# Optimization experiments

Hardware: AMD Instinct MI355X
Metric: run time of the kernel (lower is better)

## Reference

```python
import jax, jax.numpy as jnp
import numpy as np

B, S, D, H = 2, 2048, 2048, 16
DH = D // H  # 128


def _rope(x, cos, sin):
    # Faithful to the source: x is (B, H, S, Dh) (already transposed), and the
    # original apply_rotary_emb slices freqs_cis[:, :H, :] and broadcasts over
    # the S axis -> rotation angle depends on head index (source quirk).
    h = x.shape[1]
    c = cos[:, :h, :][:, :, None, :]  # (1, H, 1, Dh/2)
    s = sin[:, :h, :][:, :, None, :]
    half = x.shape[-1] // 2
    re, im = x[..., :half], x[..., half:]
    return jnp.concatenate([re * c - im * s, re * s + im * c], axis=-1)


def setup_inputs() -> dict:
    key = jax.random.key(0)
    k0, k1, k2 = jax.random.split(key, 3)
    x = jax.random.normal(k0, (B, S, D), jnp.float32)
    Wqkv = jax.random.normal(k1, (D, 3 * D), jnp.float32) / np.float32(np.sqrt(D))
    bqkv = jnp.zeros((3 * D,), jnp.float32)
    Wout = jax.random.normal(k2, (D, D), jnp.float32) / np.float32(np.sqrt(D))
    bout = jnp.zeros((D,), jnp.float32)
    # standard RoPE frequency table, stored as cos/sin (unit-modulus complex)
    inv_freq = 1.0 / (10000.0 ** (np.arange(0, DH // 2, dtype=np.float32) / (DH // 2)))
    ang = np.outer(np.arange(S, dtype=np.float32), inv_freq)  # (S, Dh/2)
    freqs_cos = jnp.asarray(np.cos(ang)[None], jnp.float32)   # (1, S, Dh/2)
    freqs_sin = jnp.asarray(np.sin(ang)[None], jnp.float32)
    mask = jnp.triu(jnp.ones((S, S), bool), 1)[None, None]    # causal, True = masked
    return {"x": x, "Wqkv": Wqkv, "bqkv": bqkv, "Wout": Wout, "bout": bout,
            "freqs_cos": freqs_cos, "freqs_sin": freqs_sin, "mask": mask}


def reference(x, Wqkv, bqkv, Wout, bout, freqs_cos, freqs_sin, mask):
    b, s, d = x.shape
    scale = DH ** (-0.5)
    qkv = x @ Wqkv + bqkv                                   # (B, S, 3D)
    q, k, v = jnp.split(qkv, 3, axis=-1)
    to_heads = lambda t: t.reshape(b, s, H, DH).transpose(0, 2, 1, 3)  # (B,H,S,Dh)
    q, k, v = to_heads(q), to_heads(k), to_heads(v)
    q = _rope(q, freqs_cos, freqs_sin)
    k = _rope(k, freqs_cos, freqs_sin)
    scores = jnp.einsum('bhqd,bhkd->bhqk', q, k) * scale
    scores = jnp.where(mask, -jnp.inf, scores)
    p = jax.nn.softmax(scores, axis=-1)                     # dropout p=0 (eval)
    out = jnp.einsum('bhqk,bhkd->bhqd', p, v)
    out = out.transpose(0, 2, 1, 3).reshape(b, s, d)
    return out @ Wout + bout
```

## Files before the change

kernel.cpp:

```cpp
#include <hip/hip_runtime.h>

#define S_ 2048
#define D_ 2048
#define H_ 16
#define DH_ 128

typedef __attribute__((ext_vector_type(8))) short short8;
typedef __attribute__((ext_vector_type(4))) float f32x4;
typedef __attribute__((ext_vector_type(8))) unsigned short ushort8;
typedef __attribute__((ext_vector_type(4))) unsigned short ushort4v;

__device__ __forceinline__ unsigned short f2bf(float f) {
  unsigned int u;
  __builtin_memcpy(&u, &f, 4);
  unsigned int lsb = (u >> 16) & 1u;
  u += 0x7fffu + lsb;
  return (unsigned short)(u >> 16);
}

__device__ __forceinline__ void gload_lds16(const void* g, void* l) {
  __builtin_amdgcn_global_load_lds(
      (const __attribute__((address_space(1))) unsigned int*)g,
      (__attribute__((address_space(3))) unsigned int*)l, 16, 0, 0);
}

template <int N> __device__ __forceinline__ void vmwait() {
  if constexpr (N == 8)      asm volatile("s_waitcnt vmcnt(8)" ::: "memory");
  else if constexpr (N == 6) asm volatile("s_waitcnt vmcnt(6)" ::: "memory");
  else if constexpr (N == 4) asm volatile("s_waitcnt vmcnt(4)" ::: "memory");
  else if constexpr (N == 3) asm volatile("s_waitcnt vmcnt(3)" ::: "memory");
  else if constexpr (N == 2) asm volatile("s_waitcnt vmcnt(2)" ::: "memory");
  else                       asm volatile("s_waitcnt vmcnt(0)" ::: "memory");
}

#define FENCE_ asm volatile("" ::: "memory")
#define BAR_ { FENCE_; __builtin_amdgcn_s_barrier(); FENCE_; }

__global__ void k_convert_x(const float* __restrict__ x, unsigned short* __restrict__ xb) {
  int idx = blockIdx.x * 256 + threadIdx.x;
  const float4* xv = (const float4*)x;
  float4 a = xv[(size_t)idx * 2];
  float4 b = xv[(size_t)idx * 2 + 1];
  ushort8 o;
  o[0] = f2bf(a.x); o[1] = f2bf(a.y); o[2] = f2bf(a.z); o[3] = f2bf(a.w);
  o[4] = f2bf(b.x); o[5] = f2bf(b.y); o[6] = f2bf(b.z); o[7] = f2bf(b.w);
  *(ushort8*)(xb + (size_t)idx * 8) = o;
}

__global__ void k_prep_w(const float* __restrict__ W, const float* __restrict__ cosb,
                         const float* __restrict__ sinb, unsigned short* __restrict__ WT,
                         int Nw, int rot_limit) {
  __shared__ float tile[32][129];
  const int t = threadIdx.x;
  const int kt = blockIdx.x * 32, nt = blockIdx.y * 128;
#pragma unroll
  for (int i = 0; i < 4; ++i) {
    int q = i * 256 + t;
    int kl = q >> 5, cq = q & 31;
    float4 v = *(const float4*)(W + (size_t)(kt + kl) * Nw + nt + cq * 4);
    tile[kl][cq * 4 + 0] = v.x; tile[kl][cq * 4 + 1] = v.y;
    tile[kl][cq * 4 + 2] = v.z; tile[kl][cq * 4 + 3] = v.w;
  }
  __syncthreads();
  const bool rot = nt < rot_limit;
#pragma unroll
  for (int i = 0; i < 16; ++i) {
    int f = i * 256 + t;
    int kl = f & 31, nl = f >> 5;
    int ng = nt + nl;
    float val;
    if (rot) {
      int i0 = nl & 63;
      int h = (ng & 2047) >> 7;
      float c = cosb[h * 64 + i0], sn = sinb[h * 64 + i0];
      float re = tile[kl][i0], im = tile[kl][i0 + 64];
      val = (nl < 64) ? (re * c - im * sn) : (re * sn + im * c);
    } else {
      val = tile[kl][nl];
    }
    WT[(size_t)ng * 2048 + kt + kl] = f2bf(val);
  }
}

template <int NF, int MODE>
__global__ __launch_bounds__(512, 2) void k_ms(
    const unsigned short* __restrict__ A, const unsigned short* __restrict__ Bt,
    const float* __restrict__ bias,
    unsigned short* __restrict__ Qb, unsigned short* __restrict__ Kb,
    unsigned short* __restrict__ Vt, float* __restrict__ Co) {
  constexpr int BN = NF * 64;
  constexpr int NT = 32;
  constexpr int BBASE = 65536;
  constexpr int BSZ = BN * 128;
  __shared__ unsigned char lds[BBASE + 3 * BSZ];

  const int tid = threadIdx.x, l = tid & 63, w = tid >> 6;
  const int wm = w >> 2, wn = w & 3;
  const int nwg = gridDim.x;
  const int bid = blockIdx.x;
  const int swz = (bid & 7) * (nwg >> 3) + (bid >> 3);
  const int tm = (swz & 15) * 256;
  const int tn = (swz >> 4) * BN;

  const int sslot = (l & 7) ^ (l >> 3);
  const unsigned short* aB = A + (size_t)(tm + (l >> 3)) * 2048 + sslot * 8;
  const unsigned short* bB = Bt + (size_t)(tn + (l >> 3)) * 2048 + sslot * 8;
  const int xg = ((l >> 4) ^ (l & 7)) << 4;
  const int afo = (wm * 128 + (l & 15)) * 128 + xg;
  const int bfo = (wn * (NF * 16) + (l & 15)) * 128 + xg;

  f32x4 acc[8][NF] = {};
  short8 af[8], bf[2 * NF];

#define SAF_(ab_, u_) {                                                         \
  _Pragma("unroll") for (int i_ = 0; i_ < 4; ++i_) {                            \
    int c_ = w + i_ * 8;                                                        \
    gload_lds16(aB + (size_t)(c_ * 8) * 2048 + (u_) * 64,                       \
                lds + (ab_) + c_ * 1024); } }
#define SBF_(bs_, u_) {                                                         \
  _Pragma("unroll") for (int i_ = 0; i_ < NF; ++i_) {                           \
    int c_ = w + i_ * 8;                                                        \
    gload_lds16(bB + (size_t)(c_ * 8) * 2048 + (u_) * 64,                       \
                lds + (bs_) + c_ * 1024); } }

#define RDA2_(ab_, mh_) {                                                       \
  _Pragma("unroll") for (int m_ = 0; m_ < 4; ++m_) {                            \
    unsigned a_ = (ab_) + afo + ((mh_) * 4 + m_) * 2048;                        \
    af[m_]     = *(const short8*)(lds + a_);                                    \
    af[4 + m_] = *(const short8*)(lds + (a_ ^ 64)); } }
#define RDB2_(bb_) {                                                            \
  _Pragma("unroll") for (int n_ = 0; n_ < NF; ++n_) {                           \
    unsigned a_ = (bb_) + bfo + n_ * 2048;                                      \
    bf[n_]      = *(const short8*)(lds + a_);                                   \
    bf[NF + n_] = *(const short8*)(lds + (a_ ^ 64)); } }

#define MMF_(mh_) { __builtin_amdgcn_s_setprio(1);                              \
  _Pragma("unroll") for (int kk_ = 0; kk_ < 2; ++kk_)                           \
  _Pragma("unroll") for (int m_ = 0; m_ < 4; ++m_)                              \
  _Pragma("unroll") for (int n_ = 0; n_ < NF; ++n_)                             \
    acc[(mh_) * 4 + m_][n_] = __builtin_amdgcn_mfma_f32_16x16x32_bf16(          \
        af[kk_ * 4 + m_], bf[kk_ * NF + n_], acc[(mh_) * 4 + m_][n_], 0, 0, 0); \
  __builtin_amdgcn_s_setprio(0); }

  SAF_(0u, 0); SBF_(BBASE, 0); SBF_(BBASE + BSZ, 1);
  vmwait<NF>(); BAR_;

  int bcur = 0, bstg = 2;
#pragma unroll 1
  for (int v = 0; v < NT; ++v) {
    const unsigned ab = (unsigned)(v & 1) * 32768u;
    const unsigned an = (unsigned)((v + 1) & 1) * 32768u;
    const unsigned bb = BBASE + (unsigned)bcur * BSZ;
    const unsigned bs = BBASE + (unsigned)bstg * BSZ;
    RDB2_(bb);
    RDA2_(ab, 0);
    if (v + 1 < NT) SAF_(an, v + 1);
    MMF_(0);
    RDA2_(ab, 1);
    if (v + 2 < NT) SBF_(bs, v + 2);
    MMF_(1);
    if (v < NT - 2) { vmwait<NF>(); } else { vmwait<0>(); }
    BAR_;
    bcur = (bcur == 2) ? 0 : bcur + 1;
    bstg = (bstg == 2) ? 0 : bstg + 1;
  }
#undef SAF_
#undef SBF_
#undef RDA2_
#undef RDB2_
#undef MMF_

  const int ln = l & 15, rb4 = (l >> 4) << 2;
#pragma unroll
  for (int m = 0; m < 8; ++m) {
    int rbase = tm + wm * 128 + m * 16 + rb4;
#pragma unroll
    for (int n = 0; n < NF; ++n) {
      int colg = tn + wn * (NF * 16) + n * 16 + ln;
      float bv = bias[colg];
      if constexpr (MODE == 0) {
        int reg = colg >> 11;
        int h = (colg & 2047) >> 7, dh = colg & 127;
        if (reg == 2) {
          int b = rbase >> 11, s = rbase & 2047;
          ushort4v o;
#pragma unroll
          for (int j = 0; j < 4; ++j) o[j] = f2bf(acc[m][n][j] + bv);
          *(ushort4v*)(Vt + ((size_t)(b * H_ + h) * DH_ + dh) * S_ + s) = o;
        } else {
#pragma unroll
          for (int j = 0; j < 4; ++j) {
            int r = rbase + j;
            int b = r >> 11, s = r & 2047;
            size_t off = ((size_t)(b * H_ + h) * S_ + s) * DH_ + dh;
            float v = acc[m][n][j] + bv;
            if (reg == 0) Qb[off] = f2bf(v * 0.08838834764831845f);
            else Kb[off] = f2bf(v);
          }
        }
      } else {
#pragma unroll
        for (int j = 0; j < 4; ++j)
          Co[(size_t)(rbase + j) * 2048 + colg] = acc[m][n][j] + bv;
      }
    }
  }
}

__global__ __launch_bounds__(256) void k_attn(
    const unsigned short* __restrict__ Qb, const unsigned short* __restrict__ Kb,
    const unsigned short* __restrict__ Vt, unsigned short* __restrict__ Ob) {
  __shared__ unsigned short kls[2][8192];
  __shared__ unsigned short vls[2][8192];
  __shared__ unsigned short pls[4096];
  const int t = threadIdx.x, l = t & 63, w = t >> 6;
  const int pairi = blockIdx.x, bh = blockIdx.y;
  const int b = bh >> 4, h = bh & 15;
  const int rb = (l >> 4) << 2;
  const unsigned short* Qp = Qb + (size_t)bh * S_ * DH_;
  const unsigned short* Kp = Kb + (size_t)bh * S_ * DH_;
  const unsigned short* Vp = Vt + (size_t)bh * DH_ * S_;

#pragma unroll 1
  for (int half = 0; half < 2; ++half) {
    const int qt = half ? (31 - pairi) : pairi;
    const int qb = qt * 64;

    short8 qf[4];
    {
      int row = qb + w * 16 + (l & 15);
#pragma unroll
      for (int c = 0; c < 4; ++c)
        qf[c] = *(const short8*)(Qp + (size_t)row * 128 + c * 32 + ((l >> 4) * 8));
    }

    f32x4 o[8] = {};
    float mrow[4] = {-1e30f, -1e30f, -1e30f, -1e30f};
    float lrow[4] = {0.f, 0.f, 0.f, 0.f};

#pragma unroll
    for (int i = 0; i < 4; ++i) {
      int cid = w + i * 4;
      int krow = cid * 4 + (l >> 4);
      int kslot = (l & 15) ^ (krow & 7);
      gload_lds16(Kp + (size_t)krow * 128 + kslot * 8, &kls[0][cid * 512]);
      int vrow = cid * 8 + (l >> 3);
      int vslot = (l & 7) ^ (vrow & 7);
      gload_lds16(Vp + (size_t)vrow * S_ + vslot * 8, &vls[0][cid * 512]);
    }
    __syncthreads();

#pragma unroll 1
    for (int kvt = 0; kvt <= qt; ++kvt) {
      const int kvb = kvt * 64;
      const int cur = kvt & 1;

      if (kvt < qt) {
        const int kvb2 = kvb + 64;
#pragma unroll
        for (int i = 0; i < 4; ++i) {
          int cid = w + i * 4;
          int krow = cid * 4 + (l >> 4);
          int kslot = (l & 15) ^ (krow & 7);
          gload_lds16(Kp + (size_t)(kvb2 + krow) * 128 + kslot * 8,
                      &kls[cur ^ 1][cid * 512]);
          int vrow = cid * 8 + (l >> 3);
          int vslot = (l & 7) ^ (vrow & 7);
          gload_lds16(Vp + (size_t)vrow * S_ + kvb2 + vslot * 8,
                      &vls[cur ^ 1][cid * 512]);
        }
      }

      f32x4 sc[4];
      __builtin_amdgcn_s_setprio(1);
#pragma unroll
      for (int nb = 0; nb < 4; ++nb) {
        f32x4 sacc = {};
#pragma unroll
        for (int c = 0; c < 4; ++c) {
          int row = nb * 16 + (l & 15);
          int off = (c * 64 + ((l >> 4) * 16)) ^ ((row & 7) << 4);
          short8 kf = *(const short8*)((const char*)kls[cur] + row * 256 + off);
          sacc = __builtin_amdgcn_mfma_f32_16x16x32_bf16(qf[c], kf, sacc, 0, 0, 0);
        }
        sc[nb] = sacc;
      }
      __builtin_amdgcn_s_setprio(0);

      float xs[4][4], xm[4];
      const bool diag = (kvt == qt);
#pragma unroll
      for (int j = 0; j < 4; ++j) {
        float m0 = -1e30f;
#pragma unroll
        for (int nb = 0; nb < 4; ++nb) {
          float x = sc[nb][j];
          if (diag) {
            int kv = kvb + nb * 16 + (l & 15);
            if (kv > qb + w * 16 + rb + j) x = -1e30f;
          }
          xs[j][nb] = x;
          m0 = fmaxf(m0, x);
        }
        xm[j] = m0;
      }
#pragma unroll
      for (int msk = 8; msk >= 1; msk >>= 1)
#pragma unroll
        for (int j = 0; j < 4; ++j) xm[j] = fmaxf(xm[j], __shfl_xor(xm[j], msk));

      bool grow = false;
#pragma unroll
      for (int j = 0; j < 4; ++j) grow |= (xm[j] > mrow[j] + 8.f);
      if (__any(grow)) {
        float fsc[4];
#pragma unroll
        for (int j = 0; j < 4; ++j) {
          float nm = fmaxf(mrow[j], xm[j]);
          fsc[j] = __expf(mrow[j] - nm);
          mrow[j] = nm;
        }
#pragma unroll
        for (int d = 0; d < 8; ++d) {
          o[d][0] *= fsc[0]; o[d][1] *= fsc[1]; o[d][2] *= fsc[2]; o[d][3] *= fsc[3];
        }
#pragma unroll
        for (int j = 0; j < 4; ++j) lrow[j] *= fsc[j];
      }
      float rs[4];
#pragma unroll
      for (int j = 0; j < 4; ++j) {
        float s = 0.f;
#pragma unroll
        for (int nb = 0; nb < 4; ++nb) {
          float p = __expf(xs[j][nb] - mrow[j]);
          xs[j][nb] = p;
          s += p;
        }
        rs[j] = s;
      }
#pragma unroll
      for (int msk = 8; msk >= 1; msk >>= 1)
#pragma unroll
        for (int j = 0; j < 4; ++j) rs[j] += __shfl_xor(rs[j], msk);
#pragma unroll
      for (int j = 0; j < 4; ++j) lrow[j] += rs[j];

#pragma unroll
      for (int j = 0; j < 4; ++j) {
        int prow = rb + j;
#pragma unroll
        for (int nb = 0; nb < 4; ++nb) {
          int colb = (nb * 16 + (l & 15)) * 2;
          *(unsigned short*)((char*)pls + w * 2048 + prow * 128 +
                             (colb ^ ((prow & 7) << 4))) = f2bf(xs[j][nb]);
        }
      }
      __syncthreads();

      __builtin_amdgcn_s_setprio(1);
#pragma unroll
      for (int kc = 0; kc < 2; ++kc) {
        int prow = l & 15;
        int poff = (kc * 64 + ((l >> 4) * 16)) ^ ((prow & 7) << 4);
        short8 pa = *(const short8*)((const char*)pls + w * 2048 + prow * 128 + poff);
#pragma unroll
        for (int d = 0; d < 8; ++d) {
          int vrow = d * 16 + (l & 15);
          int voff = (kc * 64 + ((l >> 4) * 16)) ^ ((vrow & 7) << 4);
          short8 vf = *(const short8*)((const char*)vls[cur] + vrow * 128 + voff);
          o[d] = __builtin_amdgcn_mfma_f32_16x16x32_bf16(pa, vf, o[d], 0, 0, 0);
        }
      }
      __builtin_amdgcn_s_setprio(0);
      __syncthreads();
    }

    float inv[4];
#pragma unroll
    for (int j = 0; j < 4; ++j) inv[j] = 1.f / lrow[j];
#pragma unroll
    for (int d = 0; d < 8; ++d) {
#pragma unroll
      for (int j = 0; j < 4; ++j) {
        int s = qb + w * 16 + rb + j;
        int col = h * 128 + d * 16 + (l & 15);
        Ob[((size_t)(b * S_ + s)) * D_ + col] = f2bf(o[d][j] * inv[j]);
      }
    }
  }
}

extern "C" void kernel_launch(void* const* d_in, const int* in_sizes, int n_in,
                              void* d_out, int out_size, void* d_ws, size_t ws_size,
                              hipStream_t stream) {
  const float* x    = (const float*)d_in[0];
  const float* Wqkv = (const float*)d_in[1];
  const float* bqkv = (const float*)d_in[2];
  const float* Wout = (const float*)d_in[3];
  const float* bout = (const float*)d_in[4];
  const float* fcos = (const float*)d_in[5];
  const float* fsin = (const float*)d_in[6];
  float* out = (float*)d_out;

  char* ws = (char*)d_ws;
  unsigned short* xbf   = (unsigned short*)(ws);
  unsigned short* wqkvT = (unsigned short*)(ws + 16777216);
  unsigned short* woutT = (unsigned short*)(ws + 41943040);
  unsigned short* Qb    = (unsigned short*)(ws + 50331648);
  unsigned short* Kb    = Qb + 8388608;
  unsigned short* Vtb   = Kb + 8388608;
  unsigned short* Ob    = xbf;

  hipLaunchKernelGGL(k_convert_x, dim3(4096), dim3(256), 0, stream, x, xbf);
  hipLaunchKernelGGL(k_prep_w, dim3(64, 48), dim3(256), 0, stream,
                     Wqkv, fcos, fsin, wqkvT, 6144, 4096);
  hipLaunchKernelGGL(k_prep_w, dim3(64, 16), dim3(256), 0, stream,
                     Wout, fcos, fsin, woutT, 2048, 0);
  hipLaunchKernelGGL((k_ms<3, 0>), dim3(512), dim3(512), 0, stream,
                     xbf, wqkvT, bqkv, Qb, Kb, Vtb, (float*)nullptr);
  hipLaunchKernelGGL(k_attn, dim3(16, 32), dim3(256), 0, stream, Qb, Kb, Vtb, Ob);
  hipLaunchKernelGGL((k_ms<2, 1>), dim3(256), dim3(512), 0, stream,
                     Ob, woutT, bout, (unsigned short*)nullptr,
                     (unsigned short*)nullptr, (unsigned short*)nullptr, out);
}
```

Before: 278.0 us.

## Transpose attention score MFMA so each lane owns one query row

After: 249.6 us. -10.2%, faster.

```diff
diff --git a/kernel.cpp b/kernel.cpp
--- a/kernel.cpp
+++ b/kernel.cpp
@@ -122,7 +122,6 @@
     int c_ = w + i_ * 8;                                                        \
     gload_lds16(bB + (size_t)(c_ * 8) * 2048 + (u_) * 64,                       \
                 lds + (bs_) + c_ * 1024); } }
-
 #define RDA2_(ab_, mh_) {                                                       \
   _Pragma("unroll") for (int m_ = 0; m_ < 4; ++m_) {                            \
     unsigned a_ = (ab_) + afo + ((mh_) * 4 + m_) * 2048;                        \
@@ -133,7 +132,6 @@
     unsigned a_ = (bb_) + bfo + n_ * 2048;                                      \
     bf[n_]      = *(const short8*)(lds + a_);                                   \
     bf[NF + n_] = *(const short8*)(lds + (a_ ^ 64)); } }
-
 #define MMF_(mh_) { __builtin_amdgcn_s_setprio(1);                              \
   _Pragma("unroll") for (int kk_ = 0; kk_ < 2; ++kk_)                           \
   _Pragma("unroll") for (int m_ = 0; m_ < 4; ++m_)                              \
@@ -214,9 +212,11 @@
   __shared__ unsigned short vls[2][8192];
   __shared__ unsigned short pls[4096];
   const int t = threadIdx.x, l = t & 63, w = t >> 6;
-  const int pairi = blockIdx.x, bh = blockIdx.y;
+  const int id = blockIdx.x;
+  const int pairi = id >> 5, bh = id & 31;
   const int b = bh >> 4, h = bh & 15;
-  const int rb = (l >> 4) << 2;
+  const int lq = l & 15, lg = l >> 4;
+  const int rb = lg << 2;
   const unsigned short* Qp = Qb + (size_t)bh * S_ * DH_;
   const unsigned short* Kp = Kb + (size_t)bh * S_ * DH_;
   const unsigned short* Vp = Vt + (size_t)bh * DH_ * S_;
@@ -225,18 +225,15 @@
   for (int half = 0; half < 2; ++half) {
     const int qt = half ? (31 - pairi) : pairi;
     const int qb = qt * 64;
+    const int qrow = qb + w * 16 + lq;
 
     short8 qf[4];
-    {
-      int row = qb + w * 16 + (l & 15);
-#pragma unroll
-      for (int c = 0; c < 4; ++c)
-        qf[c] = *(const short8*)(Qp + (size_t)row * 128 + c * 32 + ((l >> 4) * 8));
-    }
+#pragma unroll
+    for (int c = 0; c < 4; ++c)
+      qf[c] = *(const short8*)(Qp + (size_t)qrow * 128 + c * 32 + lg * 8);
 
     f32x4 o[8] = {};
-    float mrow[4] = {-1e30f, -1e30f, -1e30f, -1e30f};
-    float lrow[4] = {0.f, 0.f, 0.f, 0.f};
+    float m = -1e30f, lsum = 0.f;
 
 #pragma unroll
     for (int i = 0; i < 4; ++i) {
@@ -278,96 +275,73 @@
         f32x4 sacc = {};
 #pragma unroll
         for (int c = 0; c < 4; ++c) {
-          int row = nb * 16 + (l & 15);
-          int off = (c * 64 + ((l >> 4) * 16)) ^ ((row & 7) << 4);
+          int row = nb * 16 + lq;
+          int off = (c * 64 + (lg * 16)) ^ ((row & 7) << 4);
           short8 kf = *(const short8*)((const char*)kls[cur] + row * 256 + off);
-          sacc = __builtin_amdgcn_mfma_f32_16x16x32_bf16(qf[c], kf, sacc, 0, 0, 0);
+          sacc = __builtin_amdgcn_mfma_f32_16x16x32_bf16(kf, qf[c], sacc, 0, 0, 0);
         }
         sc[nb] = sacc;
       }
       __builtin_amdgcn_s_setprio(0);
 
-      float xs[4][4], xm[4];
+      float xs[4][4];
+      float xm = -1e30f;
       const bool diag = (kvt == qt);
 #pragma unroll
-      for (int j = 0; j < 4; ++j) {
-        float m0 = -1e30f;
-#pragma unroll
-        for (int nb = 0; nb < 4; ++nb) {
-          float x = sc[nb][j];
-          if (diag) {
-            int kv = kvb + nb * 16 + (l & 15);
-            if (kv > qb + w * 16 + rb + j) x = -1e30f;
-          }
-          xs[j][nb] = x;
-          m0 = fmaxf(m0, x);
-        }
-        xm[j] = m0;
-      }
-#pragma unroll
-      for (int msk = 8; msk >= 1; msk >>= 1)
-#pragma unroll
-        for (int j = 0; j < 4; ++j) xm[j] = fmaxf(xm[j], __shfl_xor(xm[j], msk));
-
-      bool grow = false;
-#pragma unroll
-      for (int j = 0; j < 4; ++j) grow |= (xm[j] > mrow[j] + 8.f);
-      if (__any(grow)) {
-        float fsc[4];
-#pragma unroll
-        for (int j = 0; j < 4; ++j) {
-          float nm = fmaxf(mrow[j], xm[j]);
-          fsc[j] = __expf(mrow[j] - nm);
-          mrow[j] = nm;
-        }
+      for (int nb = 0; nb < 4; ++nb)
+#pragma unroll
+        for (int r = 0; r < 4; ++r) {
+          float x = sc[nb][r];
+          if (diag && (kvb + nb * 16 + rb + r > qrow)) x = -1e30f;
+          xs[nb][r] = x;
+          xm = fmaxf(xm, x);
+        }
+      xm = fmaxf(xm, __shfl_xor(xm, 16));
+      xm = fmaxf(xm, __shfl_xor(xm, 32));
+
+      if (__any(xm > m + 8.f)) {
+        float nm = fmaxf(m, xm);
+        float f = __expf(m - nm);
+        m = nm; lsum *= f;
+        float fj[4];
+#pragma unroll
+        for (int j = 0; j < 4; ++j) fj[j] = __shfl(f, (l & 48) | (rb + j));
 #pragma unroll
         for (int d = 0; d < 8; ++d) {
-          o[d][0] *= fsc[0]; o[d][1] *= fsc[1]; o[d][2] *= fsc[2]; o[d][3] *= fsc[3];
-        }
-#pragma unroll
-        for (int j = 0; j < 4; ++j) lrow[j] *= fsc[j];
-      }
-      float rs[4];
-#pragma unroll
-      for (int j = 0; j < 4; ++j) {
-        float s = 0.f;
-#pragma unroll
-        for (int nb = 0; nb < 4; ++nb) {
-          float p = __expf(xs[j][nb] - mrow[j]);
-          xs[j][nb] = p;
+          o[d][0] *= fj[0]; o[d][1] *= fj[1]; o[d][2] *= fj[2]; o[d][3] *= fj[3];
+        }
+      }
+      float s = 0.f;
+#pragma unroll
+      for (int nb = 0; nb < 4; ++nb)
+#pragma unroll
+        for (int r = 0; r < 4; ++r) {
+          float p = __expf(xs[nb][r] - m);
+          xs[nb][r] = p;
           s += p;
         }
-        rs[j] = s;
-      }
-#pragma unroll
-      for (int msk = 8; msk >= 1; msk >>= 1)
-#pragma unroll
-        for (int j = 0; j < 4; ++j) rs[j] += __shfl_xor(rs[j], msk);
-#pragma unroll
-      for (int j = 0; j < 4; ++j) lrow[j] += rs[j];
-
-#pragma unroll
-      for (int j = 0; j < 4; ++j) {
-        int prow = rb + j;
-#pragma unroll
-        for (int nb = 0; nb < 4; ++nb) {
-          int colb = (nb * 16 + (l & 15)) * 2;
-          *(unsigned short*)((char*)pls + w * 2048 + prow * 128 +
-                             (colb ^ ((prow & 7) << 4))) = f2bf(xs[j][nb]);
-        }
-      }
-      __syncthreads();
+      s += __shfl_xor(s, 16);
+      s += __shfl_xor(s, 32);
+      lsum += s;
+
+#pragma unroll
+      for (int nb = 0; nb < 4; ++nb) {
+        ushort4v pw;
+#pragma unroll
+        for (int r = 0; r < 4; ++r) pw[r] = f2bf(xs[nb][r]);
+        *(ushort4v*)((char*)pls + w * 2048 + lq * 128 +
+                     ((nb * 32 + lg * 8) ^ ((lq & 7) << 4))) = pw;
+      }
 
       __builtin_amdgcn_s_setprio(1);
 #pragma unroll
       for (int kc = 0; kc < 2; ++kc) {
-        int prow = l & 15;
-        int poff = (kc * 64 + ((l >> 4) * 16)) ^ ((prow & 7) << 4);
-        short8 pa = *(const short8*)((const char*)pls + w * 2048 + prow * 128 + poff);
+        short8 pa = *(const short8*)((const char*)pls + w * 2048 + lq * 128 +
+                                     ((kc * 64 + lg * 16) ^ ((lq & 7) << 4)));
 #pragma unroll
         for (int d = 0; d < 8; ++d) {
-          int vrow = d * 16 + (l & 15);
-          int voff = (kc * 64 + ((l >> 4) * 16)) ^ ((vrow & 7) << 4);
+          int vrow = d * 16 + lq;
+          int voff = (kc * 64 + (lg * 16)) ^ ((vrow & 7) << 4);
           short8 vf = *(const short8*)((const char*)vls[cur] + vrow * 128 + voff);
           o[d] = __builtin_amdgcn_mfma_f32_16x16x32_bf16(pa, vf, o[d], 0, 0, 0);
         }
@@ -376,16 +350,17 @@
       __syncthreads();
     }
 
-    float inv[4];
-#pragma unroll
-    for (int j = 0; j < 4; ++j) inv[j] = 1.f / lrow[j];
+    float inv = 1.f / lsum;
+    float invj[4];
+#pragma unroll
+    for (int j = 0; j < 4; ++j) invj[j] = __shfl(inv, (l & 48) | (rb + j));
 #pragma unroll
     for (int d = 0; d < 8; ++d) {
 #pragma unroll
       for (int j = 0; j < 4; ++j) {
         int s = qb + w * 16 + rb + j;
-        int col = h * 128 + d * 16 + (l & 15);
-        Ob[((size_t)(b * S_ + s)) * D_ + col] = f2bf(o[d][j] * inv[j]);
+        int col = h * 128 + d * 16 + lq;
+        Ob[((size_t)(b * S_ + s)) * D_ + col] = f2bf(o[d][j] * invj[j]);
       }
     }
   }
@@ -419,7 +394,7 @@
                      Wout, fcos, fsin, woutT, 2048, 0);
   hipLaunchKernelGGL((k_ms<3, 0>), dim3(512), dim3(512), 0, stream,
                      xbf, wqkvT, bqkv, Qb, Kb, Vtb, (float*)nullptr);
-  hipLaunchKernelGGL(k_attn, dim3(16, 32), dim3(256), 0, stream, Qb, Kb, Vtb, Ob);
+  hipLaunchKernelGGL(k_attn, dim3(512), dim3(256), 0, stream, Qb, Kb, Vtb, Ob);
   hipLaunchKernelGGL((k_ms<2, 1>), dim3(256), dim3(512), 0, stream,
                      Ob, woutT, bout, (unsigned short*)nullptr,
                      (unsigned short*)nullptr, (unsigned short*)nullptr, out);
```
